# Performance work log

Measured on AMD Instinct MI355X. Metric: run time of the kernel, lower is better.

Reference implementation:

```python
import jax, jax.numpy as jnp
import numpy as np

LOC_SCOPE = 3.0
LOC_BIN_SIZE = 0.5
NUM_HEAD_BIN = 12
PER_LOC_BIN = int(LOC_SCOPE / LOC_BIN_SIZE) * 2  # 12
REG_C = PER_LOC_BIN * 4 + 1 + NUM_HEAD_BIN * 2 + 3  # 76


def decode_bbox_target(roi, reg, anchor):
    # roi: (M, 3) point centers; reg: (M, 76); anchor: (3,)
    b = PER_LOC_BIN
    f32 = reg.dtype
    x_bin = jnp.argmax(reg[:, 0:b], axis=1)
    z_bin = jnp.argmax(reg[:, b:2 * b], axis=1)
    pos_x = x_bin.astype(f32) * LOC_BIN_SIZE + LOC_BIN_SIZE / 2 - LOC_SCOPE
    pos_z = z_bin.astype(f32) * LOC_BIN_SIZE + LOC_BIN_SIZE / 2 - LOC_SCOPE
    # fine xz residual: gather residual of the argmax bin (batch_dims=1 gather)
    x_res = jnp.take_along_axis(reg[:, 2 * b:3 * b], x_bin[:, None], axis=1)[:, 0] * LOC_BIN_SIZE
    z_res = jnp.take_along_axis(reg[:, 3 * b:4 * b], z_bin[:, None], axis=1)[:, 0] * LOC_BIN_SIZE
    pos_x = pos_x + x_res
    pos_z = pos_z + z_res
    start = 4 * b
    # y by direct offset (get_y_by_bin=False)
    pos_y = roi[:, 1] + reg[:, start]
    start = start + 1
    # heading: coarse bin argmax + fine residual gather (get_ry_fine=False)
    ry_bin = jnp.argmax(reg[:, start:start + NUM_HEAD_BIN], axis=1)
    ry_res_norm = jnp.take_along_axis(
        reg[:, start + NUM_HEAD_BIN:start + 2 * NUM_HEAD_BIN], ry_bin[:, None], axis=1)[:, 0]
    angle_per_class = 2.0 * np.pi / NUM_HEAD_BIN
    ry = (ry_bin.astype(f32) * angle_per_class + ry_res_norm * (angle_per_class / 2)) % (2.0 * np.pi)
    ry = jnp.where(ry > np.pi, ry - 2.0 * np.pi, ry)
    # size: residual around anchor
    hwl = reg[:, start + 2 * NUM_HEAD_BIN:start + 2 * NUM_HEAD_BIN + 3] * anchor + anchor
    # roi has 3 cols -> no rotate_pc_along_y branch; shift x,z by roi center
    box = jnp.concatenate([
        (pos_x + roi[:, 0])[:, None],
        pos_y[:, None],
        (pos_z + roi[:, 2])[:, None],
        hwl,
        ry[:, None],
    ], axis=1)  # (M, 7)
    return box


def setup_inputs() -> dict:
    key = jax.random.key(0)
    k1, k2, k3 = jax.random.split(key, 3)
    B, N = 8, 131072
    rpn_scores = jax.random.normal(k1, (B, N), dtype=jnp.float32)
    rpn_reg = jax.random.normal(k2, (B, N, REG_C), dtype=jnp.float32)
    xyz = jax.random.normal(k3, (B, N, 3), dtype=jnp.float32) * 20.0
    anchor_size = jnp.array([1.52563191462, 1.62856739989, 3.88311640418], dtype=jnp.float32)
    return {"rpn_scores": rpn_scores, "rpn_reg": rpn_reg, "xyz": xyz, "anchor_size": anchor_size}


def reference(rpn_scores, rpn_reg, xyz, anchor_size):
    B, N, C = rpn_reg.shape
    props = decode_bbox_target(xyz.reshape(-1, 3), rpn_reg.reshape(-1, C), anchor_size)
    props = props.reshape(B, N, 7)
    # post_process: lift y to box top-center (y + h/2)
    props = jnp.concatenate([props[..., :1], props[..., 1:2] + props[..., 3:4] / 2, props[..., 2:]], axis=-1)
    # score-descending ordering of proposals (per batch row)
    order = jnp.argsort(-rpn_scores, axis=1)  # (B, N)
    boxes = jnp.take_along_axis(props, order[..., None], axis=1)
    scores = jnp.take_along_axis(rpn_scores, order, axis=1)
    # pack boxes+scores: (B, N, 8)
    return jnp.concatenate([boxes, scores[..., None]], axis=-1)
```

## Files before the change

### kernel.cpp

```cpp
#include <hip/hip_runtime.h>
#include <math.h>

#define N_PER   131072
#define NBATCH  8
#define REGC    76
#define TOTAL   (NBATCH * N_PER)
#define TILE    4096
#define NBLKSEG 32
#define BINS    256

__device__ __forceinline__ unsigned desc_key(float f) {
    unsigned u = __float_as_uint(f);
    return (u & 0x80000000u) ? u : ~(u | 0x80000000u);
}

__global__ __launch_bounds__(256) void decode_kernel(
    const float* __restrict__ scores, const float* __restrict__ reg,
    const float* __restrict__ xyz, const float* __restrict__ anchor,
    float* __restrict__ boxes8, unsigned* __restrict__ keyA,
    unsigned* __restrict__ payA)
{
    int p = blockIdx.x * 256 + threadIdx.x;
    const float* r = reg + (size_t)p * REGC;
    const float4* r4 = (const float4*)r;

    float4 q0 = r4[0],  q1 = r4[1],  q2 = r4[2];
    float4 q3 = r4[3],  q4 = r4[4],  q5 = r4[5];
    float4 s0 = r4[12], s1 = r4[13], s2 = r4[14], s3 = r4[15];
    float4 tt = r4[18];

    float xa[12] = {q0.x,q0.y,q0.z,q0.w, q1.x,q1.y,q1.z,q1.w, q2.x,q2.y,q2.z,q2.w};
    float za[12] = {q3.x,q3.y,q3.z,q3.w, q4.x,q4.y,q4.z,q4.w, q5.x,q5.y,q5.z,q5.w};
    float ra[12] = {s0.y,s0.z,s0.w, s1.x,s1.y,s1.z,s1.w, s2.x,s2.y,s2.z,s2.w, s3.x};

    int xb = 0; float xm = xa[0];
#pragma unroll
    for (int c = 1; c < 12; ++c) { if (xa[c] > xm) { xm = xa[c]; xb = c; } }
    int zb = 0; float zm = za[0];
#pragma unroll
    for (int c = 1; c < 12; ++c) { if (za[c] > zm) { zm = za[c]; zb = c; } }
    int yb = 0; float ym = ra[0];
#pragma unroll
    for (int c = 1; c < 12; ++c) { if (ra[c] > ym) { ym = ra[c]; yb = c; } }

    float x_res  = r[24 + xb];
    float z_res  = r[36 + zb];
    float ry_res = r[61 + yb];

    float rx = xyz[(size_t)p * 3 + 0];
    float ryy = xyz[(size_t)p * 3 + 1];
    float rz = xyz[(size_t)p * 3 + 2];
    float a0 = anchor[0], a1 = anchor[1], a2 = anchor[2];

    const float APC    = (float)(2.0 * M_PI / 12.0);
    const float HAPC   = (float)(M_PI / 12.0);
    const float TWO_PI = (float)(2.0 * M_PI);
    const float PI_F   = (float)M_PI;

    float vry = __fadd_rn(__fmul_rn((float)yb, APC), __fmul_rn(ry_res, HAPC));
    float m = fmodf(vry, TWO_PI);
    if (m < 0.0f) m += TWO_PI;
    if (m > PI_F) m -= TWO_PI;

    float h = tt.y * a0 + a0;
    float w = tt.z * a1 + a1;
    float l = tt.w * a2 + a2;

    float ox = (((float)xb * 0.5f + 0.25f - 3.0f) + x_res * 0.5f) + rx;
    float oz = (((float)zb * 0.5f + 0.25f - 3.0f) + z_res * 0.5f) + rz;
    float oy = (ryy + s0.x) + h * 0.5f;

    float sc = scores[p];

    float4* ob = (float4*)(boxes8 + (size_t)p * 8);
    ob[0] = make_float4(ox, oy, oz, h);
    ob[1] = make_float4(w, l, m, sc);

    keyA[p] = desc_key(sc);
    payA[p] = (unsigned)(p & (N_PER - 1));
}

__global__ __launch_bounds__(256) void hist_kernel(
    const unsigned* __restrict__ keyIn, unsigned* __restrict__ hist, int shift)
{
    __shared__ unsigned h[BINS];
    int tid = threadIdx.x;
    h[tid] = 0;
    __syncthreads();
    int seg = blockIdx.y, blk = blockIdx.x;
    const unsigned* k = keyIn + (size_t)seg * N_PER + (size_t)blk * TILE;
#pragma unroll
    for (int c = 0; c < TILE / 256; ++c) {
        unsigned d = (k[c * 256 + tid] >> shift) & 255u;
        atomicAdd(&h[d], 1u);
    }
    __syncthreads();
    hist[(size_t)(seg * BINS + tid) * NBLKSEG + blk] = h[tid];
}

__global__ __launch_bounds__(256) void scan_kernel(unsigned* __restrict__ hist)
{
    int seg = blockIdx.x, bin = threadIdx.x;
    unsigned* hp = hist + (size_t)(seg * BINS + bin) * NBLKSEG;
    unsigned run = 0;
#pragma unroll
    for (int blk = 0; blk < NBLKSEG; ++blk) {
        unsigned c = hp[blk];
        hp[blk] = run;
        run += c;
    }
    __shared__ unsigned sc[BINS];
    sc[bin] = run;
    __syncthreads();
    for (int off = 1; off < BINS; off <<= 1) {
        unsigned v = (bin >= off) ? sc[bin - off] : 0u;
        __syncthreads();
        sc[bin] += v;
        __syncthreads();
    }
    unsigned excl = sc[bin] - run;
#pragma unroll
    for (int blk = 0; blk < NBLKSEG; ++blk) hp[blk] += excl;
}

__global__ __launch_bounds__(256) void scatter_kernel(
    const unsigned* __restrict__ keyIn, const unsigned* __restrict__ payIn,
    unsigned* __restrict__ keyOut, unsigned* __restrict__ payOut,
    const unsigned* __restrict__ hist, int shift)
{
    __shared__ unsigned offs[BINS];
    __shared__ unsigned running[BINS];
    __shared__ unsigned whist[4][BINS];
    int tid = threadIdx.x;
    int seg = blockIdx.y, blk = blockIdx.x;
    int wave = tid >> 6, lane = tid & 63;
    unsigned long long lmask = (1ull << lane) - 1ull;

    offs[tid] = hist[(size_t)(seg * BINS + tid) * NBLKSEG + blk];
    running[tid] = 0;
#pragma unroll
    for (int w2 = 0; w2 < 4; ++w2) whist[w2][tid] = 0;

    const unsigned* ki = keyIn + (size_t)seg * N_PER + (size_t)blk * TILE;
    const unsigned* pi = payIn + (size_t)seg * N_PER + (size_t)blk * TILE;
    unsigned* ko = keyOut + (size_t)seg * N_PER;
    unsigned* po = payOut + (size_t)seg * N_PER;

    for (int c = 0; c < TILE / 256; ++c) {
        __syncthreads();
        unsigned key = ki[c * 256 + tid];
        unsigned pay = pi[c * 256 + tid];
        unsigned d = (key >> shift) & 255u;
        unsigned long long peers = ~0ull;
#pragma unroll
        for (int b = 0; b < 8; ++b) {
            unsigned long long vote = __ballot((d >> b) & 1u);
            peers &= ((d >> b) & 1u) ? vote : ~vote;
        }
        unsigned rank = (unsigned)__popcll(peers & lmask);
        unsigned cnt  = (unsigned)__popcll(peers);
        if (rank == 0) whist[wave][d] = cnt;
        __syncthreads();
        unsigned prefix = running[d];
#pragma unroll
        for (int w2 = 0; w2 < 4; ++w2) { if (w2 < wave) prefix += whist[w2][d]; }
        unsigned pos = offs[d] + prefix + rank;
        ko[pos] = key;
        po[pos] = pay;
        __syncthreads();
        unsigned sum = whist[0][tid] + whist[1][tid] + whist[2][tid] + whist[3][tid];
        running[tid] += sum;
        whist[0][tid] = 0; whist[1][tid] = 0; whist[2][tid] = 0; whist[3][tid] = 0;
    }
}

__global__ __launch_bounds__(256) void gather_kernel(
    const float* __restrict__ boxes8, const unsigned* __restrict__ pay,
    float* __restrict__ out)
{
    int g = blockIdx.x * 256 + threadIdx.x;
    int row = g >> 1, half = g & 1;
    int b = row >> 17;
    unsigned i = pay[row];
    const float4* src = (const float4*)(boxes8 + ((size_t)((b << 17) | (int)i)) * 8);
    float4 v = src[half];
    ((float4*)(out + (size_t)row * 8))[half] = v;
}

extern "C" void kernel_launch(void* const* d_in, const int* in_sizes, int n_in,
                              void* d_out, int out_size, void* d_ws, size_t ws_size,
                              hipStream_t stream)
{
    const float* scores = (const float*)d_in[0];
    const float* reg    = (const float*)d_in[1];
    const float* xyz    = (const float*)d_in[2];
    const float* anchor = (const float*)d_in[3];
    float* out = (float*)d_out;

    char* ws = (char*)d_ws;
    float*    boxes8 = (float*)ws;
    size_t    off    = (size_t)TOTAL * 8 * sizeof(float);
    unsigned* keyA = (unsigned*)(ws + off); off += (size_t)TOTAL * 4;
    unsigned* payA = (unsigned*)(ws + off); off += (size_t)TOTAL * 4;
    unsigned* keyB = (unsigned*)(ws + off); off += (size_t)TOTAL * 4;
    unsigned* payB = (unsigned*)(ws + off); off += (size_t)TOTAL * 4;
    unsigned* hist = (unsigned*)(ws + off); off += (size_t)NBATCH * BINS * NBLKSEG * 4;
    (void)ws_size; (void)in_sizes; (void)n_in; (void)out_size;

    decode_kernel<<<TOTAL / 256, 256, 0, stream>>>(scores, reg, xyz, anchor,
                                                   boxes8, keyA, payA);

    unsigned *ka = keyA, *pa = payA, *kb = keyB, *pb = payB;
    for (int pass = 0; pass < 4; ++pass) {
        int shift = pass * 8;
        hist_kernel<<<dim3(NBLKSEG, NBATCH), 256, 0, stream>>>(ka, hist, shift);
        scan_kernel<<<NBATCH, 256, 0, stream>>>(hist);
        scatter_kernel<<<dim3(NBLKSEG, NBATCH), 256, 0, stream>>>(ka, pa, kb, pb,
                                                                  hist, shift);
        unsigned* t;
        t = ka; ka = kb; kb = t;
        t = pa; pa = pb; pb = t;
    }

    gather_kernel<<<(TOTAL * 2) / 256, 256, 0, stream>>>(boxes8, pa, out);
}
```

Before: 589.1 us.

## Restructure radix sort: fold scan into scatter, local shared-memory reorder, templated passes

Removes the separate scan kernel by having each scatter block recompute its bin offsets from a compact 16-bit histogram. The scatter now ranks a 2048-key tile in one go, reorders keys and payloads in shared memory, then writes them out in bin-contiguous runs, which should coalesce the global writes. Pass 0 reads scores directly instead of keys written by decode, and the last pass skips writing keys. Blocks are interleaved across batches and the tile is halved to get more blocks, at the cost of more shared memory per block and redundant histogram prefix reads.

```diff
diff --git a/kernel.cpp b/kernel.cpp
--- a/kernel.cpp
+++ b/kernel.cpp
@@ -5,9 +5,11 @@
 #define NBATCH  8
 #define REGC    76
 #define TOTAL   (NBATCH * N_PER)
-#define TILE    4096
-#define NBLKSEG 32
+#define TILE    2048
+#define NBLKSEG (N_PER / TILE)
 #define BINS    256
+#define SCTH    512
+#define CHUNKS  (TILE / SCTH)
 
 __device__ __forceinline__ unsigned desc_key(float f) {
     unsigned u = __float_as_uint(f);
@@ -17,8 +19,7 @@
 __global__ __launch_bounds__(256) void decode_kernel(
     const float* __restrict__ scores, const float* __restrict__ reg,
     const float* __restrict__ xyz, const float* __restrict__ anchor,
-    float* __restrict__ boxes8, unsigned* __restrict__ keyA,
-    unsigned* __restrict__ payA)
+    float* __restrict__ boxes8)
 {
     int p = blockIdx.x * 256 + threadIdx.x;
     const float* r = reg + (size_t)p * REGC;
@@ -75,82 +76,104 @@
     float4* ob = (float4*)(boxes8 + (size_t)p * 8);
     ob[0] = make_float4(ox, oy, oz, h);
     ob[1] = make_float4(w, l, m, sc);
-
-    keyA[p] = desc_key(sc);
-    payA[p] = (unsigned)(p & (N_PER - 1));
-}
-
+}
+
+template<int PASS>
 __global__ __launch_bounds__(256) void hist_kernel(
-    const unsigned* __restrict__ keyIn, unsigned* __restrict__ hist, int shift)
+    const float* __restrict__ scores, const unsigned* __restrict__ keyIn,
+    unsigned short* __restrict__ hist)
 {
     __shared__ unsigned h[BINS];
     int tid = threadIdx.x;
     h[tid] = 0;
     __syncthreads();
-    int seg = blockIdx.y, blk = blockIdx.x;
-    const unsigned* k = keyIn + (size_t)seg * N_PER + (size_t)blk * TILE;
+    int id = blockIdx.x;
+    int seg = id & 7, blk = id >> 3;
+    size_t base = (size_t)seg * N_PER + (size_t)blk * TILE;
 #pragma unroll
     for (int c = 0; c < TILE / 256; ++c) {
-        unsigned d = (k[c * 256 + tid] >> shift) & 255u;
-        atomicAdd(&h[d], 1u);
-    }
-    __syncthreads();
-    hist[(size_t)(seg * BINS + tid) * NBLKSEG + blk] = h[tid];
-}
-
-__global__ __launch_bounds__(256) void scan_kernel(unsigned* __restrict__ hist)
-{
-    int seg = blockIdx.x, bin = threadIdx.x;
-    unsigned* hp = hist + (size_t)(seg * BINS + bin) * NBLKSEG;
-    unsigned run = 0;
-#pragma unroll
-    for (int blk = 0; blk < NBLKSEG; ++blk) {
-        unsigned c = hp[blk];
-        hp[blk] = run;
-        run += c;
-    }
-    __shared__ unsigned sc[BINS];
-    sc[bin] = run;
-    __syncthreads();
-    for (int off = 1; off < BINS; off <<= 1) {
-        unsigned v = (bin >= off) ? sc[bin - off] : 0u;
-        __syncthreads();
-        sc[bin] += v;
-        __syncthreads();
-    }
-    unsigned excl = sc[bin] - run;
-#pragma unroll
-    for (int blk = 0; blk < NBLKSEG; ++blk) hp[blk] += excl;
-}
-
-__global__ __launch_bounds__(256) void scatter_kernel(
+        unsigned key;
+        if (PASS == 0) key = desc_key(scores[base + c * 256 + tid]);
+        else           key = keyIn[base + c * 256 + tid];
+        atomicAdd(&h[(key >> (PASS * 8)) & 255u], 1u);
+    }
+    __syncthreads();
+    hist[(size_t)(seg * NBLKSEG + blk) * BINS + tid] = (unsigned short)h[tid];
+}
+
+template<int PASS>
+__global__ __launch_bounds__(512) void scatter_kernel(
+    const float* __restrict__ scores,
     const unsigned* __restrict__ keyIn, const unsigned* __restrict__ payIn,
     unsigned* __restrict__ keyOut, unsigned* __restrict__ payOut,
-    const unsigned* __restrict__ hist, int shift)
-{
+    const unsigned short* __restrict__ hist)
+{
+    __shared__ unsigned whist[CHUNKS * 8][BINS];
+    __shared__ unsigned skey[TILE];
+    __shared__ unsigned spay[TILE];
     __shared__ unsigned offs[BINS];
-    __shared__ unsigned running[BINS];
-    __shared__ unsigned whist[4][BINS];
-    int tid = threadIdx.x;
-    int seg = blockIdx.y, blk = blockIdx.x;
-    int wave = tid >> 6, lane = tid & 63;
-    unsigned long long lmask = (1ull << lane) - 1ull;
-
-    offs[tid] = hist[(size_t)(seg * BINS + tid) * NBLKSEG + blk];
-    running[tid] = 0;
-#pragma unroll
-    for (int w2 = 0; w2 < 4; ++w2) whist[w2][tid] = 0;
-
-    const unsigned* ki = keyIn + (size_t)seg * N_PER + (size_t)blk * TILE;
-    const unsigned* pi = payIn + (size_t)seg * N_PER + (size_t)blk * TILE;
-    unsigned* ko = keyOut + (size_t)seg * N_PER;
-    unsigned* po = payOut + (size_t)seg * N_PER;
-
-    for (int c = 0; c < TILE / 256; ++c) {
-        __syncthreads();
-        unsigned key = ki[c * 256 + tid];
-        unsigned pay = pi[c * 256 + tid];
-        unsigned d = (key >> shift) & 255u;
+    __shared__ unsigned lexcl[BINS];
+    __shared__ unsigned wsum[4];
+
+    const int tid  = threadIdx.x;
+    const int wave = tid >> 6, lane = tid & 63;
+    const unsigned long long lmask = (1ull << lane) - 1ull;
+    const int id  = blockIdx.x;
+    const int seg = id & 7, blk = id >> 3;
+    const size_t segbase = (size_t)seg * N_PER;
+    const int gbase = blk * TILE;
+
+    unsigned my_pref = 0, my_tot = 0;
+    if (tid < BINS) {
+        const unsigned short* hp = hist + (size_t)(seg * NBLKSEG) * BINS + tid;
+        unsigned pref = 0, tot = 0;
+#pragma unroll
+        for (int b = 0; b < NBLKSEG; ++b) {
+            unsigned c = hp[(size_t)b * BINS];
+            tot += c;
+            if (b < blk) pref += c;
+        }
+        my_pref = pref; my_tot = tot;
+    } else {
+        int z = tid - BINS;
+        unsigned* wf = &whist[0][0];
+#pragma unroll
+        for (int k = 0; k < CHUNKS * 8; ++k) wf[k * BINS + z] = 0;
+    }
+    __syncthreads();
+
+    unsigned my_base = 0;
+    if (tid < BINS) {
+        unsigned v = my_tot;
+#pragma unroll
+        for (int o = 1; o < 64; o <<= 1) {
+            unsigned n = __shfl_up(v, o, 64);
+            if (lane >= o) v += n;
+        }
+        if (lane == 63) wsum[wave] = v;
+        my_base = v - my_tot;
+    }
+    __syncthreads();
+    if (tid < BINS) {
+        unsigned add = 0;
+#pragma unroll
+        for (int w2 = 0; w2 < 4; ++w2) { if (w2 < wave) add += wsum[w2]; }
+        offs[tid] = my_base + add + my_pref;
+    }
+
+    unsigned kr[CHUNKS], pr[CHUNKS], dr[CHUNKS], rr[CHUNKS];
+#pragma unroll
+    for (int c = 0; c < CHUNKS; ++c) {
+        int idx = c * SCTH + tid;
+        unsigned key, pay;
+        if (PASS == 0) {
+            key = desc_key(scores[segbase + gbase + idx]);
+            pay = (unsigned)(gbase + idx);
+        } else {
+            key = keyIn[segbase + gbase + idx];
+            pay = payIn[segbase + gbase + idx];
+        }
+        unsigned d = (key >> (PASS * 8)) & 255u;
         unsigned long long peers = ~0ull;
 #pragma unroll
         for (int b = 0; b < 8; ++b) {
@@ -158,19 +181,56 @@
             peers &= ((d >> b) & 1u) ? vote : ~vote;
         }
         unsigned rank = (unsigned)__popcll(peers & lmask);
-        unsigned cnt  = (unsigned)__popcll(peers);
-        if (rank == 0) whist[wave][d] = cnt;
-        __syncthreads();
-        unsigned prefix = running[d];
-#pragma unroll
-        for (int w2 = 0; w2 < 4; ++w2) { if (w2 < wave) prefix += whist[w2][d]; }
-        unsigned pos = offs[d] + prefix + rank;
-        ko[pos] = key;
-        po[pos] = pay;
-        __syncthreads();
-        unsigned sum = whist[0][tid] + whist[1][tid] + whist[2][tid] + whist[3][tid];
-        running[tid] += sum;
-        whist[0][tid] = 0; whist[1][tid] = 0; whist[2][tid] = 0; whist[3][tid] = 0;
+        if (rank == 0) whist[c * 8 + wave][d] = (unsigned)__popcll(peers);
+        kr[c] = key; pr[c] = pay; dr[c] = d; rr[c] = rank;
+    }
+    __syncthreads();
+
+    unsigned my_ltot = 0, my_lpart = 0;
+    if (tid < BINS) {
+        unsigned run = 0;
+#pragma unroll
+        for (int i = 0; i < CHUNKS * 8; ++i) {
+            unsigned v = whist[i][tid];
+            whist[i][tid] = run;
+            run += v;
+        }
+        my_ltot = run;
+        unsigned v = run;
+#pragma unroll
+        for (int o = 1; o < 64; o <<= 1) {
+            unsigned n = __shfl_up(v, o, 64);
+            if (lane >= o) v += n;
+        }
+        if (lane == 63) wsum[wave] = v;
+        my_lpart = v - my_ltot;
+    }
+    __syncthreads();
+    if (tid < BINS) {
+        unsigned add = 0;
+#pragma unroll
+        for (int w2 = 0; w2 < 4; ++w2) { if (w2 < wave) add += wsum[w2]; }
+        lexcl[tid] = my_lpart + add;
+    }
+    __syncthreads();
+
+#pragma unroll
+    for (int c = 0; c < CHUNKS; ++c) {
+        unsigned j = lexcl[dr[c]] + whist[c * 8 + wave][dr[c]] + rr[c];
+        skey[j] = kr[c];
+        spay[j] = pr[c];
+    }
+    __syncthreads();
+
+#pragma unroll
+    for (int c = 0; c < CHUNKS; ++c) {
+        unsigned j = (unsigned)(c * SCTH + tid);
+        unsigned key = skey[j];
+        unsigned pay = spay[j];
+        unsigned d = (key >> (PASS * 8)) & 255u;
+        unsigned g = offs[d] + (j - lexcl[d]);
+        if (PASS < 3) keyOut[segbase + g] = key;
+        payOut[segbase + g] = pay;
     }
 }
 
@@ -178,13 +238,17 @@
     const float* __restrict__ boxes8, const unsigned* __restrict__ pay,
     float* __restrict__ out)
 {
-    int g = blockIdx.x * 256 + threadIdx.x;
-    int row = g >> 1, half = g & 1;
-    int b = row >> 17;
+    int id = blockIdx.x;
+    int seg = id & 7;
+    int bi  = id >> 3;
+    int t   = threadIdx.x;
+    int rowInSeg = bi * 128 + (t >> 1);
+    int half = t & 1;
+    size_t row = (size_t)seg * N_PER + rowInSeg;
     unsigned i = pay[row];
-    const float4* src = (const float4*)(boxes8 + ((size_t)((b << 17) | (int)i)) * 8);
+    const float4* src = (const float4*)(boxes8 + ((size_t)seg * N_PER + i) * 8);
     float4 v = src[half];
-    ((float4*)(out + (size_t)row * 8))[half] = v;
+    ((float4*)(out + row * 8))[half] = v;
 }
 
 extern "C" void kernel_launch(void* const* d_in, const int* in_sizes, int n_in,
@@ -204,23 +268,26 @@
     unsigned* payA = (unsigned*)(ws + off); off += (size_t)TOTAL * 4;
     unsigned* keyB = (unsigned*)(ws + off); off += (size_t)TOTAL * 4;
     unsigned* payB = (unsigned*)(ws + off); off += (size_t)TOTAL * 4;
-    unsigned* hist = (unsigned*)(ws + off); off += (size_t)NBATCH * BINS * NBLKSEG * 4;
+    unsigned short* hist = (unsigned short*)(ws + off);
+    off += (size_t)NBATCH * NBLKSEG * BINS * sizeof(unsigned short);
     (void)ws_size; (void)in_sizes; (void)n_in; (void)out_size;
 
-    decode_kernel<<<TOTAL / 256, 256, 0, stream>>>(scores, reg, xyz, anchor,
-                                                   boxes8, keyA, payA);
-
-    unsigned *ka = keyA, *pa = payA, *kb = keyB, *pb = payB;
-    for (int pass = 0; pass < 4; ++pass) {
-        int shift = pass * 8;
-        hist_kernel<<<dim3(NBLKSEG, NBATCH), 256, 0, stream>>>(ka, hist, shift);
-        scan_kernel<<<NBATCH, 256, 0, stream>>>(hist);
-        scatter_kernel<<<dim3(NBLKSEG, NBATCH), 256, 0, stream>>>(ka, pa, kb, pb,
-                                                                  hist, shift);
-        unsigned* t;
-        t = ka; ka = kb; kb = t;
-        t = pa; pa = pb; pb = t;
-    }
-
-    gather_kernel<<<(TOTAL * 2) / 256, 256, 0, stream>>>(boxes8, pa, out);
-}
+    decode_kernel<<<TOTAL / 256, 256, 0, stream>>>(scores, reg, xyz, anchor, boxes8);
+
+    const int NG = NBATCH * NBLKSEG;
+
+    hist_kernel<0><<<NG, 256, 0, stream>>>(scores, nullptr, hist);
+    scatter_kernel<0><<<NG, SCTH, 0, stream>>>(scores, nullptr, nullptr,
+                                               keyB, payB, hist);
+    hist_kernel<1><<<NG, 256, 0, stream>>>(nullptr, keyB, hist);
+    scatter_kernel<1><<<NG, SCTH, 0, stream>>>(nullptr, keyB, payB,
+                                               keyA, payA, hist);
+    hist_kernel<2><<<NG, 256, 0, stream>>>(nullptr, keyA, hist);
+    scatter_kernel<2><<<NG, SCTH, 0, stream>>>(nullptr, keyA, payA,
+                                               keyB, payB, hist);
+    hist_kernel<3><<<NG, 256, 0, stream>>>(nullptr, keyB, hist);
+    scatter_kernel<3><<<NG, SCTH, 0, stream>>>(nullptr, keyB, payB,
+                                               nullptr, payA, hist);
+
+    gather_kernel<<<NBATCH * (N_PER / 128), 256, 0, stream>>>(boxes8, payA, out);
+}
```

Measured after the change: 523.3 us. 11.2% less time.
